# Kernel optimization log

Hardware: AMD Instinct MI355X
Metric: run time of the kernel (lower is better)

Reference implementation:

```python
import jax, jax.numpy as jnp
import numpy as np

N_NODES = 50000
NUM_FEAT = 128
HIDDEN = 128
NUM_OUT = 40
E_REG = 800000
E_EGO = 1600000


def setup_inputs() -> dict:
    key = jax.random.key(0)
    ks = jax.random.split(key, 12)
    def lin(k, fi, fo):
        s = 1.0 / np.sqrt(fi)
        return jax.random.uniform(k, (fi, fo), jnp.float32, -s, s)
    return {
        "x_in": jax.random.normal(ks[0], (N_NODES, NUM_FEAT), jnp.float32),
        "edge_index_in": jax.random.randint(ks[1], (2, E_REG), 0, N_NODES, jnp.int64),
        "ego_edge_index": jax.random.randint(ks[2], (2, E_EGO), 0, N_NODES, jnp.int64),
        "W1": lin(ks[3], NUM_FEAT, NUM_FEAT),
        "b1": jnp.zeros((NUM_FEAT,), jnp.float32),
        "Wg1": lin(ks[4], NUM_FEAT, HIDDEN),
        "bg1": jnp.zeros((HIDDEN,), jnp.float32),
        "W2": lin(ks[5], HIDDEN, HIDDEN),
        "b2": jnp.zeros((HIDDEN,), jnp.float32),
        "Wg2": lin(ks[6], HIDDEN, NUM_OUT),
        "bg2": jnp.zeros((NUM_OUT,), jnp.float32),
    }


def _do_conv(x, ego_ei, n):
    # spmm with all-ones values over the union of all ego edge lists:
    # out[row] = sum_{(row,col) in ego edges} x[col]; then * (1/numNodes)
    out = jax.ops.segment_sum(x[ego_ei[1]], ego_ei[0], num_segments=n)
    return out * (1.0 / n)


def _gin_agg(x, ei, n):
    # PyG GINConv (eps=0): x_i + sum_{(j,i) in E} x_j
    return x + jax.ops.segment_sum(x[ei[0]], ei[1], num_segments=n)


def reference(x_in, edge_index_in, ego_edge_index, W1, b1, Wg1, bg1, W2, b2, Wg2, bg2):
    n = x_in.shape[0]
    # Layer 1: Ego conv + Linear, relu, GIN, relu
    x = _do_conv(x_in, ego_edge_index, n)
    x = x @ W1 + b1
    x = jax.nn.relu(x)
    x = _gin_agg(x, edge_index_in, n) @ Wg1 + bg1
    x = jax.nn.relu(x)
    # Layer 2: Ego conv + Linear, relu, GIN (no final relu)
    x = _do_conv(x, ego_edge_index, n)
    x = x @ W2 + b2
    x = jax.nn.relu(x)
    x = _gin_agg(x, edge_index_in, n) @ Wg2 + bg2
    return jax.nn.log_softmax(x, axis=1)
```

## Files before the change

kernel.cpp:

```cpp
#include <hip/hip_runtime.h>
#include <hip/hip_bf16.h>
#include <math.h>


#define FEAT 128
#define BSH 6
#define CHUNK 8192
#define CAPB 4096

typedef unsigned short ushort_t;
typedef unsigned int uint_t;

__device__ inline float bflo(uint_t u) { return __uint_as_float(u << 16); }
__device__ inline float bfhi(uint_t u) { return __uint_as_float(u & 0xFFFF0000u); }
__device__ inline ushort_t f2bf(float f) {
    union { float f; uint_t u; } c; c.f = f;
    uint_t u = c.u;
    return (ushort_t)((u + 0x7FFFu + ((u >> 16) & 1u)) >> 16);
}
__device__ inline uint_t pack2(float lo, float hi) {
    return (uint_t)f2bf(lo) | ((uint_t)f2bf(hi) << 16);
}

__global__ __launch_bounds__(256) void cast_k(
    const float* __restrict__ in, ushort_t* __restrict__ out, int n4)
{
    int i = blockIdx.x * 256 + threadIdx.x;
    if (i >= n4) return;
    float4 v = ((const float4*)in)[i];
    ushort4 o;
    o.x = f2bf(v.x); o.y = f2bf(v.y); o.z = f2bf(v.z); o.w = f2bf(v.w);
    ((ushort4*)out)[i] = o;
}

__global__ __launch_bounds__(256) void chunkhist_k(
    const int* __restrict__ dst, int E, uint_t* __restrict__ cnts)
{
    __shared__ uint_t cnt[1024];
    int tid = threadIdx.x;
    int e0 = blockIdx.x * CHUNK;
    int n = min(CHUNK, E - e0);
    for (int b = tid; b < 1024; b += 256) cnt[b] = 0;
    __syncthreads();
    for (int i = tid; i < n; i += 256)
        atomicAdd(&cnt[dst[e0 + i] >> BSH], 1u);
    __syncthreads();
    uint_t* o = cnts + (size_t)blockIdx.x * 1024;
    for (int b = tid; b < 1024; b += 256) o[b] = cnt[b];
}

__global__ __launch_bounds__(1024) void chunkscan_k(
    const uint_t* __restrict__ cnts, int nch,
    int* __restrict__ bstart, uint_t* __restrict__ base)
{
    __shared__ uint_t s[1024];
    int b = threadIdx.x;
    uint_t tot = 0;
    for (int c = 0; c < nch; ++c) tot += cnts[(size_t)c * 1024 + b];
    s[b] = tot; __syncthreads();
    for (int d = 1; d < 1024; d <<= 1) {
        uint_t v = (b >= d) ? s[b - d] : 0;
        __syncthreads();
        s[b] += v;
        __syncthreads();
    }
    uint_t excl = s[b] - tot;
    bstart[b] = (int)excl;
    if (b == 1023) bstart[1024] = (int)s[1023];
    uint_t run = excl;
    for (int c = 0; c < nch; ++c) {
        base[(size_t)c * 1024 + b] = run;
        run += cnts[(size_t)c * 1024 + b];
    }
}

__global__ __launch_bounds__(256) void binscat_k(
    const int* __restrict__ dst, const int* __restrict__ src, int E,
    const uint_t* __restrict__ basearr, uint_t* __restrict__ staged)
{
    __shared__ uint_t cnt[1024];
    __shared__ uint_t sc[1024];
    __shared__ uint_t gbase[1024];
    __shared__ uint_t part[256];
    __shared__ uint_t srt[CHUNK];

    int tid = threadIdx.x;
    int e0 = blockIdx.x * CHUNK;
    int n = min(CHUNK, E - e0);

    for (int i = tid; i < 1024; i += 256) cnt[i] = 0;
    __syncthreads();

    for (int i = tid; i < n; i += 256)
        atomicAdd(&cnt[dst[e0 + i] >> BSH], 1u);
    __syncthreads();

    uint_t a0 = cnt[4*tid], a1 = cnt[4*tid+1], a2 = cnt[4*tid+2], a3 = cnt[4*tid+3];
    uint_t gs = a0 + a1 + a2 + a3;
    part[tid] = gs; __syncthreads();
    for (int d = 1; d < 256; d <<= 1) {
        uint_t v = (tid >= d) ? part[tid - d] : 0;
        __syncthreads();
        part[tid] += v;
        __syncthreads();
    }
    uint_t b4 = part[tid] - gs;
    sc[4*tid]   = b4;
    sc[4*tid+1] = b4 + a0;
    sc[4*tid+2] = b4 + a0 + a1;
    sc[4*tid+3] = b4 + a0 + a1 + a2;
    __syncthreads();

    const uint_t* gb = basearr + (size_t)blockIdx.x * 1024;
    for (int b = tid; b < 1024; b += 256) gbase[b] = gb[b];
    for (int b = tid; b < 1024; b += 256) cnt[b] = sc[b];
    __syncthreads();

    for (int i = tid; i < n; i += 256) {
        int d = dst[e0 + i];
        int s = src[e0 + i];
        uint_t b = (uint_t)(d >> BSH);
        uint_t p = atomicAdd(&cnt[b], 1u);
        srt[p] = (b << 22) | ((uint_t)s << 6) | (uint_t)(d & 63);
    }
    __syncthreads();

    for (int i = tid; i < n; i += 256) {
        uint_t v = srt[i];
        uint_t b = v >> 22;
        staged[gbase[b] + ((uint_t)i - sc[b])] = v & 0x3FFFFFu;
    }
}

__global__ __launch_bounds__(256) void csrfin_k(
    const uint_t* __restrict__ staged, const int* __restrict__ bstart,
    int* __restrict__ deg, int* __restrict__ start, int* __restrict__ col, int N)
{
    __shared__ int ldeg[64], loff[64], lcur[64];
    __shared__ uint_t buf[CAPB];
    int tid = threadIdx.x;
    int b = blockIdx.x;
    int lo = bstart[b];
    int n = bstart[b + 1] - lo;

    if (tid < 64) ldeg[tid] = 0;
    __syncthreads();
    for (int i = tid; i < n; i += 256)
        atomicAdd(&ldeg[staged[lo + i] & 63], 1);
    __syncthreads();
    if (tid == 0) {
        int r = 0;
        for (int j = 0; j < 64; ++j) { loff[j] = r; r += ldeg[j]; }
    }
    __syncthreads();
    if (tid < 64) {
        int node = (b << BSH) + tid;
        if (node < N) { deg[node] = ldeg[tid]; start[node] = lo + loff[tid]; }
        lcur[tid] = loff[tid];
    }
    __syncthreads();
    for (int i = tid; i < n; i += 256) {
        uint_t v = staged[lo + i];
        int p = atomicAdd(&lcur[v & 63], 1);
        if (p < CAPB) buf[p] = v >> 6;
    }
    __syncthreads();
    for (int i = tid; i < n; i += 256) col[lo + i] = (int)buf[i];
}

template<bool SELF>
__global__ __launch_bounds__(256) void csr_agg_bf_k(
    const ushort_t* __restrict__ x, const int* __restrict__ col,
    const int* __restrict__ start, const int* __restrict__ deg,
    ushort_t* __restrict__ out, int N, float scale)
{
    int w = (blockIdx.x * 256 + threadIdx.x) >> 6;
    if (w >= N) return;
    int lane = threadIdx.x & 63;
    int quarter = lane >> 4;
    int q = lane & 15;

    int s0 = start[w];
    int d  = deg[w];

    float a0=0.f,a1=0.f,a2=0.f,a3=0.f,a4=0.f,a5=0.f,a6=0.f,a7=0.f;
    if (SELF && quarter == 0) {
        uint4 u = ((const uint4*)(x + (size_t)w * FEAT))[q];
        a0 = bflo(u.x); a1 = bfhi(u.x);
        a2 = bflo(u.y); a3 = bfhi(u.y);
        a4 = bflo(u.z); a5 = bfhi(u.z);
        a6 = bflo(u.w); a7 = bfhi(u.w);
    }

    int base = quarter << 4;
    for (int j = 0; j < d; j += 64) {
        int rem = d - j;
        int idx = (lane < rem) ? col[s0 + j + lane] : 0;
        int cnt = min(16, max(rem - base, 0));
#pragma unroll 4
        for (int t = 0; t < cnt; ++t) {
            int s = __shfl(idx, base + t);
            uint4 u = ((const uint4*)(x + (size_t)s * FEAT))[q];
            a0 += bflo(u.x); a1 += bfhi(u.x);
            a2 += bflo(u.y); a3 += bfhi(u.y);
            a4 += bflo(u.z); a5 += bfhi(u.z);
            a6 += bflo(u.w); a7 += bfhi(u.w);
        }
    }
    a0 += __shfl_xor(a0, 16); a0 += __shfl_xor(a0, 32);
    a1 += __shfl_xor(a1, 16); a1 += __shfl_xor(a1, 32);
    a2 += __shfl_xor(a2, 16); a2 += __shfl_xor(a2, 32);
    a3 += __shfl_xor(a3, 16); a3 += __shfl_xor(a3, 32);
    a4 += __shfl_xor(a4, 16); a4 += __shfl_xor(a4, 32);
    a5 += __shfl_xor(a5, 16); a5 += __shfl_xor(a5, 32);
    a6 += __shfl_xor(a6, 16); a6 += __shfl_xor(a6, 32);
    a7 += __shfl_xor(a7, 16); a7 += __shfl_xor(a7, 32);

    if (quarter == 0) {
        uint4 o;
        o.x = pack2(a0 * scale, a1 * scale);
        o.y = pack2(a2 * scale, a3 * scale);
        o.z = pack2(a4 * scale, a5 * scale);
        o.w = pack2(a6 * scale, a7 * scale);
        ((uint4*)(out + (size_t)w * FEAT))[q] = o;
    }
}

__global__ __launch_bounds__(256, 2) void lin128_bf_k(
    const ushort_t* __restrict__ X, const float* __restrict__ W,
    const float* __restrict__ b, ushort_t* __restrict__ Y, int nRows)
{
    __shared__ float Wl[FEAT * FEAT];
    __shared__ float Xl[32 * FEAT];
    int tid = threadIdx.x;

    const float4* Wv = (const float4*)W;
    float4* Wlv = (float4*)Wl;
#pragma unroll
    for (int i = 0; i < 16; ++i) Wlv[tid + i * 256] = Wv[tid + i * 256];

    int r0 = blockIdx.x * 32;
    const uint4* Xv = (const uint4*)(X + (size_t)r0 * FEAT);
#pragma unroll
    for (int i = 0; i < 2; ++i) {
        int fi = tid + i * 256;
        int rr = fi >> 4;
        int c8 = (fi & 15) * 8;
        float v0=0,v1=0,v2=0,v3=0,v4=0,v5=0,v6=0,v7=0;
        if (r0 + rr < nRows) {
            uint4 u = Xv[fi];
            v0 = bflo(u.x); v1 = bfhi(u.x);
            v2 = bflo(u.y); v3 = bfhi(u.y);
            v4 = bflo(u.z); v5 = bfhi(u.z);
            v6 = bflo(u.w); v7 = bfhi(u.w);
        }
        float* p = &Xl[rr * FEAT + c8];
        p[0]=v0; p[1]=v1; p[2]=v2; p[3]=v3; p[4]=v4; p[5]=v5; p[6]=v6; p[7]=v7;
    }
    __syncthreads();

    int tc = (tid & 31) * 4;
    int tr = (tid >> 5) * 4;

    float acc[4][4];
#pragma unroll
    for (int i = 0; i < 4; ++i)
#pragma unroll
        for (int j = 0; j < 4; ++j) acc[i][j] = 0.f;

    for (int k = 0; k < FEAT; ++k) {
        float4 wv = *(const float4*)&Wl[k * FEAT + tc];
        float xs[4];
#pragma unroll
        for (int i = 0; i < 4; ++i) xs[i] = Xl[(tr + i) * FEAT + k];
#pragma unroll
        for (int i = 0; i < 4; ++i) {
            acc[i][0] += xs[i] * wv.x;
            acc[i][1] += xs[i] * wv.y;
            acc[i][2] += xs[i] * wv.z;
            acc[i][3] += xs[i] * wv.w;
        }
    }

    float4 bv = *(const float4*)&b[tc];
#pragma unroll
    for (int i = 0; i < 4; ++i) {
        int r = r0 + tr + i;
        if (r < nRows) {
            float ox = fmaxf(acc[i][0] + bv.x, 0.f);
            float oy = fmaxf(acc[i][1] + bv.y, 0.f);
            float oz = fmaxf(acc[i][2] + bv.z, 0.f);
            float ow = fmaxf(acc[i][3] + bv.w, 0.f);
            ushort4 o;
            o.x = f2bf(ox); o.y = f2bf(oy); o.z = f2bf(oz); o.w = f2bf(ow);
            *(ushort4*)&Y[(size_t)r * FEAT + tc] = o;
        }
    }
}

__global__ __launch_bounds__(256) void lin40_bf_k(
    const ushort_t* __restrict__ X, const float* __restrict__ W,
    ushort_t* __restrict__ Y, int nRows)
{
    __shared__ float Wl[FEAT * 40];
    int tid = threadIdx.x;
#pragma unroll
    for (int i = 0; i < 5; ++i)
        ((float4*)Wl)[tid + i * 256] = ((const float4*)W)[tid + i * 256];
    __syncthreads();

    int lane = tid & 63;
    int wv = tid >> 6;
    int row = blockIdx.x * 4 + wv;
    if (row >= nRows) return;

    const ushort_t* xr = X + (size_t)row * FEAT;
    float acc = 0.f;
    if (lane < 40) {
        for (int k = 0; k < FEAT; ++k) {
            float xk = __uint_as_float(((uint_t)xr[k]) << 16);
            acc += xk * Wl[k * 40 + lane];
        }
        Y[(size_t)row * 40 + lane] = f2bf(acc);
    }
}

__global__ __launch_bounds__(256) void agg40_lsm_k(
    const ushort_t* __restrict__ y, const int* __restrict__ col,
    const int* __restrict__ start, const int* __restrict__ deg,
    const float* __restrict__ bias, float* __restrict__ out, int N)
{
    int w = (blockIdx.x * 256 + threadIdx.x) >> 6;
    if (w >= N) return;
    int lane = threadIdx.x & 63;
    int half = lane >> 5;
    int q = lane & 31;

    int s0 = start[w];
    int d  = deg[w];

    float ax = 0.f, ay = 0.f;
    if (half == 0 && q < 20) {
        uint_t u = ((const uint_t*)(y + (size_t)w * 40))[q];
        ax = bflo(u); ay = bfhi(u);
    }

    for (int j = 0; j < d; j += 64) {
        int rem = d - j;
        int idx = (lane < rem) ? col[s0 + j + lane] : 0;
        int cnt = half ? min(32, max(rem - 32, 0)) : min(32, rem);
        for (int t = 0; t < cnt; ++t) {
            int s = __shfl(idx, t + (half << 5));
            if (q < 20) {
                uint_t u = ((const uint_t*)(y + (size_t)s * 40))[q];
                ax += bflo(u); ay += bfhi(u);
            }
        }
    }
    ax += __shfl_xor(ax, 32);
    ay += __shfl_xor(ay, 32);

    if (q < 20) {
        ax += bias[2 * q];
        ay += bias[2 * q + 1];
    }
    float mx = (q < 20) ? fmaxf(ax, ay) : -INFINITY;
#pragma unroll
    for (int off = 1; off <= 32; off <<= 1) mx = fmaxf(mx, __shfl_xor(mx, off));
    float ex = (half == 0 && q < 20) ? (expf(ax - mx) + expf(ay - mx)) : 0.f;
#pragma unroll
    for (int off = 1; off <= 32; off <<= 1) ex += __shfl_xor(ex, off);
    float ls = logf(ex);

    if (half == 0 && q < 20) {
        float2 o = make_float2(ax - mx - ls, ay - mx - ls);
        ((float2*)(out + (size_t)w * 40))[q] = o;
    }
}


extern "C" void kernel_launch(void* const* d_in, const int* in_sizes, int n_in,
                              void* d_out, int out_size, void* d_ws, size_t ws_size,
                              hipStream_t stream) {
    const float* x_in = (const float*)d_in[0];
    const int* ei_reg = (const int*)d_in[1];
    const int* ei_ego = (const int*)d_in[2];
    const float* W1  = (const float*)d_in[3];
    const float* b1  = (const float*)d_in[4];
    const float* Wg1 = (const float*)d_in[5];
    const float* bg1 = (const float*)d_in[6];
    const float* W2  = (const float*)d_in[7];
    const float* b2  = (const float*)d_in[8];
    const float* Wg2 = (const float*)d_in[9];
    const float* bg2 = (const float*)d_in[10];
    float* out = (float*)d_out;

    const int N = in_sizes[0] / FEAT;
    const int E_reg = in_sizes[1] / 2;
    const int E_ego = in_sizes[2] / 2;
    const int NB = (N + 63) >> BSH;
    const int nch_e = (E_ego + CHUNK - 1) / CHUNK;
    const int nch_r = (E_reg + CHUNK - 1) / CHUNK;
    const float inv_n = 1.0f / (float)N;

    ushort_t* Xb  = (ushort_t*)d_ws;
    ushort_t* B0  = Xb + (size_t)N * FEAT;
    ushort_t* B1  = B0 + (size_t)N * FEAT;
    ushort_t* Y40 = B1 + (size_t)N * FEAT;
    int* colE = (int*)(Y40 + (size_t)N * 40 + ((size_t)N * 40 & 1));
    int* colR = colE + E_ego;
    uint_t* stgE = (uint_t*)(colR + E_reg);
    uint_t* stgR = stgE + E_ego;
    int* degE = (int*)(stgR + E_reg);
    int* stE  = degE + N;
    int* degR = stE + N;
    int* stR  = degR + N;
    int* bstE = stR + N;
    int* bstR = bstE + 1025;
    uint_t* cntsE = (uint_t*)(bstR + 1025);
    uint_t* cntsR = cntsE + (size_t)nch_e * 1024;
    uint_t* baseE = cntsR + (size_t)nch_r * 1024;
    uint_t* baseR = baseE + (size_t)nch_e * 1024;

    const int agg_b  = (N + 3) / 4;
    const int lin_b  = (N + 31) / 32;
    const int cast_b = ((N * FEAT / 4) + 255) / 256;

    cast_k<<<cast_b, 256, 0, stream>>>(x_in, Xb, N * FEAT / 4);
    chunkhist_k<<<nch_e, 256, 0, stream>>>(ei_ego, E_ego, cntsE);
    chunkhist_k<<<nch_r, 256, 0, stream>>>(ei_reg + E_reg, E_reg, cntsR);
    chunkscan_k<<<1, 1024, 0, stream>>>(cntsE, nch_e, bstE, baseE);
    chunkscan_k<<<1, 1024, 0, stream>>>(cntsR, nch_r, bstR, baseR);
    binscat_k<<<nch_e, 256, 0, stream>>>(ei_ego, ei_ego + E_ego, E_ego, baseE, stgE);
    binscat_k<<<nch_r, 256, 0, stream>>>(ei_reg + E_reg, ei_reg, E_reg, baseR, stgR);
    csrfin_k<<<NB, 256, 0, stream>>>(stgE, bstE, degE, stE, colE, N);
    csrfin_k<<<NB, 256, 0, stream>>>(stgR, bstR, degR, stR, colR, N);

    csr_agg_bf_k<false><<<agg_b, 256, 0, stream>>>(Xb, colE, stE, degE, B0, N, inv_n);
    lin128_bf_k<<<lin_b, 256, 0, stream>>>(B0, W1, b1, B1, N);
    csr_agg_bf_k<true><<<agg_b, 256, 0, stream>>>(B1, colR, stR, degR, B0, N, 1.0f);
    lin128_bf_k<<<lin_b, 256, 0, stream>>>(B0, Wg1, bg1, B1, N);

    csr_agg_bf_k<false><<<agg_b, 256, 0, stream>>>(B1, colE, stE, degE, B0, N, inv_n);
    lin128_bf_k<<<lin_b, 256, 0, stream>>>(B0, W2, b2, B1, N);
    lin40_bf_k<<<agg_b, 256, 0, stream>>>(B1, Wg2, Y40, N);
    agg40_lsm_k<<<agg_b, 256, 0, stream>>>(Y40, colR, stR, degR, bg2, out, N);
}
```

Measured before the change: 626.2 us.

## Replace scalar FP32 128x128 linear kernels with bf16 MFMA matrix-core kernel

Swaps the shared-memory FP32 FMA GEMM for the three 128x128 linear layers for a kernel using the 16x16x32 bf16 MFMA instruction. Weights are pre-transposed and cast to bf16 by a new small kernel, and activations are read directly into A fragments. Results go through a per-wave LDS bounce buffer so global stores are coalesced. This targets the compute cost of the dense layers, at the price of bf16 weight rounding and three extra tiny launches.

Measured after the change: 594.7 us. -5.0%, faster.

```diff
diff --git a/kernel.cpp b/kernel.cpp
--- a/kernel.cpp
+++ b/kernel.cpp
@@ -10,6 +10,8 @@
 
 typedef unsigned short ushort_t;
 typedef unsigned int uint_t;
+typedef __attribute__((ext_vector_type(8))) short short8;
+typedef __attribute__((ext_vector_type(4))) float f32x4;
 
 __device__ inline float bflo(uint_t u) { return __uint_as_float(u << 16); }
 __device__ inline float bfhi(uint_t u) { return __uint_as_float(u & 0xFFFF0000u); }
@@ -31,6 +33,14 @@
     ushort4 o;
     o.x = f2bf(v.x); o.y = f2bf(v.y); o.z = f2bf(v.z); o.w = f2bf(v.w);
     ((ushort4*)out)[i] = o;
+}
+
+__global__ __launch_bounds__(256) void wcast_k(
+    const float* __restrict__ W, ushort_t* __restrict__ Wt)
+{
+    int i = blockIdx.x * 256 + threadIdx.x;
+    int c = i >> 7, k = i & 127;
+    Wt[i] = f2bf(W[k * FEAT + c]);
 }
 
 __global__ __launch_bounds__(256) void chunkhist_k(
@@ -226,75 +236,60 @@
     }
 }
 
-__global__ __launch_bounds__(256, 2) void lin128_bf_k(
-    const ushort_t* __restrict__ X, const float* __restrict__ W,
+__global__ __launch_bounds__(256) void lin128_mfma_k(
+    const ushort_t* __restrict__ X, const ushort_t* __restrict__ Wt,
     const float* __restrict__ b, ushort_t* __restrict__ Y, int nRows)
 {
-    __shared__ float Wl[FEAT * FEAT];
-    __shared__ float Xl[32 * FEAT];
+    __shared__ ushort_t bounce[64 * FEAT];
     int tid = threadIdx.x;
-
-    const float4* Wv = (const float4*)W;
-    float4* Wlv = (float4*)Wl;
-#pragma unroll
-    for (int i = 0; i < 16; ++i) Wlv[tid + i * 256] = Wv[tid + i * 256];
-
-    int r0 = blockIdx.x * 32;
-    const uint4* Xv = (const uint4*)(X + (size_t)r0 * FEAT);
-#pragma unroll
-    for (int i = 0; i < 2; ++i) {
-        int fi = tid + i * 256;
-        int rr = fi >> 4;
-        int c8 = (fi & 15) * 8;
-        float v0=0,v1=0,v2=0,v3=0,v4=0,v5=0,v6=0,v7=0;
-        if (r0 + rr < nRows) {
-            uint4 u = Xv[fi];
-            v0 = bflo(u.x); v1 = bfhi(u.x);
-            v2 = bflo(u.y); v3 = bfhi(u.y);
-            v4 = bflo(u.z); v5 = bfhi(u.z);
-            v6 = bflo(u.w); v7 = bfhi(u.w);
+    int wid = tid >> 6, lane = tid & 63;
+    int r0 = blockIdx.x * 64 + wid * 16;
+    int la = lane & 15;
+    int lb = lane >> 4;
+
+    int arow = r0 + la;
+    if (arow >= nRows) arow = 0;
+    const ushort_t* xr = X + (size_t)arow * FEAT + lb * 8;
+    short8 afrag[4];
+#pragma unroll
+    for (int s = 0; s < 4; ++s)
+        afrag[s] = *(const short8*)(xr + s * 32);
+
+    f32x4 acc[8];
+#pragma unroll
+    for (int t = 0; t < 8; ++t) acc[t] = (f32x4){0.f, 0.f, 0.f, 0.f};
+
+#pragma unroll
+    for (int s = 0; s < 4; ++s) {
+#pragma unroll
+        for (int t = 0; t < 8; ++t) {
+            const ushort_t* wp = Wt + (size_t)(t * 16 + la) * FEAT + s * 32 + lb * 8;
+            short8 bfrag = *(const short8*)wp;
+            acc[t] = __builtin_amdgcn_mfma_f32_16x16x32_bf16(
+                afrag[s], bfrag, acc[t], 0, 0, 0);
         }
-        float* p = &Xl[rr * FEAT + c8];
-        p[0]=v0; p[1]=v1; p[2]=v2; p[3]=v3; p[4]=v4; p[5]=v5; p[6]=v6; p[7]=v7;
-    }
-    __syncthreads();
-
-    int tc = (tid & 31) * 4;
-    int tr = (tid >> 5) * 4;
-
-    float acc[4][4];
-#pragma unroll
-    for (int i = 0; i < 4; ++i)
-#pragma unroll
-        for (int j = 0; j < 4; ++j) acc[i][j] = 0.f;
-
-    for (int k = 0; k < FEAT; ++k) {
-        float4 wv = *(const float4*)&Wl[k * FEAT + tc];
-        float xs[4];
-#pragma unroll
-        for (int i = 0; i < 4; ++i) xs[i] = Xl[(tr + i) * FEAT + k];
-#pragma unroll
-        for (int i = 0; i < 4; ++i) {
-            acc[i][0] += xs[i] * wv.x;
-            acc[i][1] += xs[i] * wv.y;
-            acc[i][2] += xs[i] * wv.z;
-            acc[i][3] += xs[i] * wv.w;
+    }
+
+    ushort_t* slice = bounce + wid * (16 * FEAT);
+#pragma unroll
+    for (int t = 0; t < 8; ++t) {
+        int colc = t * 16 + la;
+        float bias = b[colc];
+#pragma unroll
+        for (int r = 0; r < 4; ++r) {
+            int row = lb * 4 + r;
+            float v = fmaxf(acc[t][r] + bias, 0.f);
+            slice[row * FEAT + colc] = f2bf(v);
         }
     }
-
-    float4 bv = *(const float4*)&b[tc];
+    __syncthreads();
 #pragma unroll
     for (int i = 0; i < 4; ++i) {
-        int r = r0 + tr + i;
-        if (r < nRows) {
-            float ox = fmaxf(acc[i][0] + bv.x, 0.f);
-            float oy = fmaxf(acc[i][1] + bv.y, 0.f);
-            float oz = fmaxf(acc[i][2] + bv.z, 0.f);
-            float ow = fmaxf(acc[i][3] + bv.w, 0.f);
-            ushort4 o;
-            o.x = f2bf(ox); o.y = f2bf(oy); o.z = f2bf(oz); o.w = f2bf(ow);
-            *(ushort4*)&Y[(size_t)r * FEAT + tc] = o;
-        }
+        int e = i * 512 + lane * 8;
+        int row = e >> 7, colc = e & 127;
+        uint4 v = *(const uint4*)(slice + e);
+        int gr = r0 + row;
+        if (gr < nRows) *(uint4*)(Y + (size_t)gr * FEAT + colc) = v;
     }
 }
 
@@ -407,7 +402,10 @@
     ushort_t* B0  = Xb + (size_t)N * FEAT;
     ushort_t* B1  = B0 + (size_t)N * FEAT;
     ushort_t* Y40 = B1 + (size_t)N * FEAT;
-    int* colE = (int*)(Y40 + (size_t)N * 40 + ((size_t)N * 40 & 1));
+    ushort_t* Wt1 = Y40 + (size_t)N * 40;
+    ushort_t* Wtg1 = Wt1 + FEAT * FEAT;
+    ushort_t* Wt2 = Wtg1 + FEAT * FEAT;
+    int* colE = (int*)(Wt2 + FEAT * FEAT);
     int* colR = colE + E_ego;
     uint_t* stgE = (uint_t*)(colR + E_reg);
     uint_t* stgR = stgE + E_ego;
@@ -423,10 +421,13 @@
     uint_t* baseR = baseE + (size_t)nch_e * 1024;
 
     const int agg_b  = (N + 3) / 4;
-    const int lin_b  = (N + 31) / 32;
+    const int mfma_b = (N + 63) / 64;
     const int cast_b = ((N * FEAT / 4) + 255) / 256;
 
     cast_k<<<cast_b, 256, 0, stream>>>(x_in, Xb, N * FEAT / 4);
+    wcast_k<<<64, 256, 0, stream>>>(W1, Wt1);
+    wcast_k<<<64, 256, 0, stream>>>(Wg1, Wtg1);
+    wcast_k<<<64, 256, 0, stream>>>(W2, Wt2);
     chunkhist_k<<<nch_e, 256, 0, stream>>>(ei_ego, E_ego, cntsE);
     chunkhist_k<<<nch_r, 256, 0, stream>>>(ei_reg + E_reg, E_reg, cntsR);
     chunkscan_k<<<1, 1024, 0, stream>>>(cntsE, nch_e, bstE, baseE);
@@ -437,12 +438,12 @@
     csrfin_k<<<NB, 256, 0, stream>>>(stgR, bstR, degR, stR, colR, N);
 
     csr_agg_bf_k<false><<<agg_b, 256, 0, stream>>>(Xb, colE, stE, degE, B0, N, inv_n);
-    lin128_bf_k<<<lin_b, 256, 0, stream>>>(B0, W1, b1, B1, N);
+    lin128_mfma_k<<<mfma_b, 256, 0, stream>>>(B0, Wt1, b1, B1, N);
     csr_agg_bf_k<true><<<agg_b, 256, 0, stream>>>(B1, colR, stR, degR, B0, N, 1.0f);
-    lin128_bf_k<<<lin_b, 256, 0, stream>>>(B0, Wg1, bg1, B1, N);
+    lin128_mfma_k<<<mfma_b, 256, 0, stream>>>(B0, Wtg1, bg1, B1, N);
 
     csr_agg_bf_k<false><<<agg_b, 256, 0, stream>>>(B1, colE, stE, degE, B0, N, inv_n);
-    lin128_bf_k<<<lin_b, 256, 0, stream>>>(B0, W2, b2, B1, N);
+    lin128_mfma_k<<<mfma_b, 256, 0, stream>>>(B0, Wt2, b2, B1, N);
     lin40_bf_k<<<agg_b, 256, 0, stream>>>(B1, Wg2, Y40, N);
     agg40_lsm_k<<<agg_b, 256, 0, stream>>>(Y40, colR, stR, degR, bg2, out, N);
 }
```
